# Performance work log

Measured on AMD Instinct MI355X. Metric: run time of the kernel, lower is better.

Reference implementation:

```python
import jax, jax.numpy as jnp
import numpy as np
import math

B, H, L, DK = 4, 12, 1024, 64
GLOBAL, LOCAL, INIT_VAL = 8, 4, 8
W = INIT_VAL + 1  # window length fed to each GRU
MAX_VAL = 1.0e12


def setup_inputs() -> dict:
    k0 = jax.random.key(0)
    ks = jax.random.split(k0, 9)
    bound = 1.0 / math.sqrt(DK)
    uni = lambda k, shape: jax.random.uniform(k, shape, jnp.float32, -bound, bound)
    return {
        "query": jax.random.normal(ks[0], (B, H, L, DK), jnp.float32),
        "key": jax.random.normal(ks[1], (B, H, L, DK), jnp.float32),
        "value": jax.random.normal(ks[2], (B, H, L, DK), jnp.float32),
        "mask": jax.random.randint(ks[3], (B, 1, L, L), 0, 2, jnp.int32),
        # per-local-head GRU parameters (torch nn.GRU layout: gates [r, z, n])
        "w_ih": uni(ks[4], (LOCAL, 3 * DK, DK)),
        "w_hh": uni(ks[5], (LOCAL, 3 * DK, DK)),
        "b_ih": uni(ks[6], (LOCAL, 3 * DK)),
        "b_hh": uni(ks[7], (LOCAL, 3 * DK)),
    }


def reference(query, key, value, mask, w_ih, w_hh, b_ih, b_hh):
    b, h, l, d_k = query.shape
    # ---- global softmax-attention heads ----
    q_g, k_g, v_g = query[:, :GLOBAL], key[:, :GLOBAL], value[:, :GLOBAL]
    scores = jnp.einsum('bhqd,bhkd->bhqk', q_g, k_g) / math.sqrt(d_k)
    scores = jnp.where(mask == 0, -MAX_VAL, scores)
    p_attn = jax.nn.softmax(scores, axis=-1)
    out_g = jnp.einsum('bhqk,bhkd->bhqd', p_attn, v_g)  # (b, GLOBAL, l, d_k)

    # ---- local heads: windowed value gather ----
    v_l = value[:, GLOBAL:]                                   # (b, LOCAL, l, d_k)
    v_pad = jnp.pad(v_l, ((0, 0), (0, 0), (0, INIT_VAL), (0, 0)))
    dist = jnp.arange(l)[:, None] + jnp.arange(W)[None, :]    # (l, W) forward window
    v_aug = v_pad[:, :, dist, :]                              # (b, LOCAL, l, W, d_k)
    x = v_aug.reshape(b * LOCAL * l, W, d_k)                  # all windows, shared by every GRU

    # ---- per-head GRU over the window; keep last hidden state ----
    def gru_last_hidden(wih, whh, bih, bhh):
        xg = jnp.einsum('ntd,gd->ntg', x, wih) + bih          # (N, W, 3*d_k), input gates precomputed
        def step(hc, xg_t):
            gh = hc @ whh.T + bhh
            xr, xz, xn = jnp.split(xg_t, 3, axis=-1)
            hr, hz, hn = jnp.split(gh, 3, axis=-1)
            r = jax.nn.sigmoid(xr + hr)
            z = jax.nn.sigmoid(xz + hz)
            n_ = jnp.tanh(xn + r * hn)
            return (1.0 - z) * n_ + z * hc, None
        h0 = jnp.zeros((x.shape[0], d_k), x.dtype)
        hT, _ = jax.lax.scan(step, h0, jnp.swapaxes(xg, 0, 1))
        return hT                                             # (N, d_k)

    hs = jax.vmap(gru_last_hidden)(w_ih, w_hh, b_ih, b_hh)    # (LOCAL, N, d_k)
    # faithful to torch cat: GRU i applied to ALL local heads -> LOCAL*LOCAL output heads
    out_l = hs.reshape(LOCAL, b, LOCAL, l, d_k).transpose(1, 0, 2, 3, 4)
    out_l = out_l.reshape(b, LOCAL * LOCAL, l, d_k)

    return jnp.concatenate([out_g, out_l], axis=1)            # (b, GLOBAL + LOCAL^2, l, d_k)
```

## Files before the change

kernel.cpp:

```cpp
#include <hip/hip_runtime.h>

#define B_  4
#define H_  12
#define L_  1024
#define DK_ 64
#define GH_ 8
#define WS_ 9

#define ATTN_LDS_BYTES (3 * 64 * 64 * 2)
#define GRU_W_OFF    0
#define GRU_XGT_OFF  24576
#define GRU_HB_OFF   81408
#define GRU_BIH_OFF  114176
#define GRU_LDS_BYTES 114944
#define XGT_STRIDE   296

#define MB_WORDS (B_ * L_ * 16)

typedef __attribute__((ext_vector_type(8))) short short8;
typedef __attribute__((ext_vector_type(4))) float f32x4;

#define MFMA_BF16(a, b, c) __builtin_amdgcn_mfma_f32_16x16x32_bf16((a), (b), (c), 0, 0, 0)

__device__ __forceinline__ unsigned short f2bf(float f) {
  unsigned int u = __builtin_bit_cast(unsigned int, f);
  u += 0x7fffu + ((u >> 16) & 1u);
  return (unsigned short)(u >> 16);
}
__device__ __forceinline__ float bf2f(unsigned short s) {
  return __builtin_bit_cast(float, ((unsigned int)s) << 16);
}
__device__ __forceinline__ short8 pack8(const float4 a, const float4 b) {
  short8 r;
  r[0] = (short)f2bf(a.x); r[1] = (short)f2bf(a.y);
  r[2] = (short)f2bf(a.z); r[3] = (short)f2bf(a.w);
  r[4] = (short)f2bf(b.x); r[5] = (short)f2bf(b.y);
  r[6] = (short)f2bf(b.z); r[7] = (short)f2bf(b.w);
  return r;
}
__device__ __forceinline__ uint4 packrow16(const float4 a, const float4 b) {
  uint4 r;
  r.x = (unsigned)f2bf(a.x) | ((unsigned)f2bf(a.y) << 16);
  r.y = (unsigned)f2bf(a.z) | ((unsigned)f2bf(a.w) << 16);
  r.z = (unsigned)f2bf(b.x) | ((unsigned)f2bf(b.y) << 16);
  r.w = (unsigned)f2bf(b.z) | ((unsigned)f2bf(b.w) << 16);
  return r;
}
__device__ __forceinline__ float xg_get(const uint2* xg3, const int wi) {
  const unsigned d = (wi & 2) ? xg3[wi >> 2].y : xg3[wi >> 2].x;
  return (wi & 1) ? __builtin_bit_cast(float, d & 0xffff0000u)
                  : __builtin_bit_cast(float, d << 16);
}

__global__ __launch_bounds__(256) void maskpack_kernel(
    const int* __restrict__ mask, unsigned long long* __restrict__ mb)
{
  const int idx = blockIdx.x * 256 + threadIdx.x;
  const int* src = mask + (size_t)idx * 64;
  unsigned long long bits = 0ull;
#pragma unroll
  for (int i = 0; i < 16; ++i) {
    const int4 m4 = *(const int4*)(src + i * 4);
    if (m4.x) bits |= 1ull << (i * 4 + 0);
    if (m4.y) bits |= 1ull << (i * 4 + 1);
    if (m4.z) bits |= 1ull << (i * 4 + 2);
    if (m4.w) bits |= 1ull << (i * 4 + 3);
  }
  mb[idx] = bits;
}

__global__ __launch_bounds__(256) void attn_kernel(
    const float* __restrict__ q, const float* __restrict__ k,
    const float* __restrict__ v, const int* __restrict__ mask,
    const unsigned long long* __restrict__ mb, const int use_bits,
    float* __restrict__ out)
{
  extern __shared__ char smc[];
  char* sK  = smc;
  char* sVT = smc + 8192;
  char* sP  = smc + 16384;

  const int tid = threadIdx.x;
  const int q0 = blockIdx.x * 64;
  const int h  = blockIdx.y;
  const int b  = blockIdx.z;

  const int w  = tid >> 6;
  const int ln = tid & 63;
  const int lg = ln >> 4;
  const int c  = ln & 15;

  const size_t hbase = ((size_t)b * H_ + h) * L_ * DK_;
  const float* kp = k + hbase;
  const float* vp = v + hbase;
  const int*   mp = mask + (size_t)b * L_ * L_;
  const unsigned long long* mbp = mb + (size_t)b * L_ * 16;

  short8 qa[2];
  {
    const float* qrow = q + hbase + (size_t)(q0 + w * 16 + c) * DK_ + lg * 8;
#pragma unroll
    for (int kt = 0; kt < 2; ++kt) {
      const float4 f0 = *(const float4*)(qrow + kt * 32);
      const float4 f1 = *(const float4*)(qrow + kt * 32 + 4);
      qa[kt] = pack8(f0, f1);
    }
  }

  char* sPw = sP + w * 2048;

  f32x4 o_[4];
#pragma unroll
  for (int nt = 0; nt < 4; ++nt) { o_[nt][0] = 0.f; o_[nt][1] = 0.f; o_[nt][2] = 0.f; o_[nt][3] = 0.f; }
  float mrun[4], lrun[4];
#pragma unroll
  for (int r = 0; r < 4; ++r) { mrun[r] = -1e30f; lrun[r] = 0.f; }

  const int rr  = tid >> 2;
  const int c16 = (tid & 3) << 4;

  float4 kreg[4], vreg[4];
  unsigned long long mreg[4];
  {
    const float* ksrc = kp + (size_t)rr * DK_ + c16;
    kreg[0] = *(const float4*)(ksrc);      kreg[1] = *(const float4*)(ksrc + 4);
    kreg[2] = *(const float4*)(ksrc + 8);  kreg[3] = *(const float4*)(ksrc + 12);
    const float* vsrc = vp + (size_t)rr * DK_ + c16;
    vreg[0] = *(const float4*)(vsrc);      vreg[1] = *(const float4*)(vsrc + 4);
    vreg[2] = *(const float4*)(vsrc + 8);  vreg[3] = *(const float4*)(vsrc + 12);
    if (use_bits) {
#pragma unroll
      for (int r = 0; r < 4; ++r)
        mreg[r] = mbp[(size_t)(q0 + w * 16 + lg * 4 + r) * 16 + 0];
    }
  }

  for (int kt0 = 0; kt0 < 16; ++kt0) {
    {
      const int kb = rr * 128 + c16 * 2;
      const int sw = (rr & 7) << 4;
      *(uint4*)(sK + ((kb) ^ sw))      = packrow16(kreg[0], kreg[1]);
      *(uint4*)(sK + ((kb + 16) ^ sw)) = packrow16(kreg[2], kreg[3]);
      const float vv[16] = {vreg[0].x, vreg[0].y, vreg[0].z, vreg[0].w,
                            vreg[1].x, vreg[1].y, vreg[1].z, vreg[1].w,
                            vreg[2].x, vreg[2].y, vreg[2].z, vreg[2].w,
                            vreg[3].x, vreg[3].y, vreg[3].z, vreg[3].w};
#pragma unroll
      for (int j = 0; j < 16; ++j) {
        const int d = c16 + j;
        *(unsigned short*)(sVT + ((d * 128 + rr * 2) ^ ((d & 7) << 4))) = f2bf(vv[j]);
      }
    }
    __syncthreads();

    unsigned long long mcur[4];
#pragma unroll
    for (int r = 0; r < 4; ++r) mcur[r] = mreg[r];
    {
      const int ktn = (kt0 + 1) & 15;
      const float* ksrc = kp + (size_t)(ktn * 64 + rr) * DK_ + c16;
      kreg[0] = *(const float4*)(ksrc);      kreg[1] = *(const float4*)(ksrc + 4);
      kreg[2] = *(const float4*)(ksrc + 8);  kreg[3] = *(const float4*)(ksrc + 12);
      const float* vsrc = vp + (size_t)(ktn * 64 + rr) * DK_ + c16;
      vreg[0] = *(const float4*)(vsrc);      vreg[1] = *(const float4*)(vsrc + 4);
      vreg[2] = *(const float4*)(vsrc + 8);  vreg[3] = *(const float4*)(vsrc + 12);
      if (use_bits) {
#pragma unroll
        for (int r = 0; r < 4; ++r)
          mreg[r] = mbp[(size_t)(q0 + w * 16 + lg * 4 + r) * 16 + ktn];
      }
    }

    f32x4 acc[4];
#pragma unroll
    for (int nt = 0; nt < 4; ++nt) {
      acc[nt][0] = 0.f; acc[nt][1] = 0.f; acc[nt][2] = 0.f; acc[nt][3] = 0.f;
#pragma unroll
      for (int kt = 0; kt < 2; ++kt) {
        const int off = (((nt * 16 + c) * 128 + kt * 64 + lg * 16) ^ ((c & 7) << 4));
        const short8 bk = __builtin_bit_cast(short8, *(const uint4*)(sK + off));
        acc[nt] = MFMA_BF16(qa[kt], bk, acc[nt]);
      }
    }

#pragma unroll
    for (int r = 0; r < 4; ++r) {
      bool k0_, k1_, k2_, k3_;
      if (use_bits) {
        const unsigned long long mword = mcur[r];
        k0_ = (mword >> (c)) & 1ull;
        k1_ = (mword >> (16 + c)) & 1ull;
        k2_ = (mword >> (32 + c)) & 1ull;
        k3_ = (mword >> (48 + c)) & 1ull;
      } else {
        const int qr = q0 + w * 16 + lg * 4 + r;
        const int* mrow = mp + (size_t)qr * L_ + kt0 * 64 + c;
        k0_ = mrow[0] != 0; k1_ = mrow[16] != 0; k2_ = mrow[32] != 0; k3_ = mrow[48] != 0;
      }
      const float s0_ = k0_ ? acc[0][r] * 0.125f : -1e12f;
      const float s1_ = k1_ ? acc[1][r] * 0.125f : -1e12f;
      const float s2_ = k2_ ? acc[2][r] * 0.125f : -1e12f;
      const float s3_ = k3_ ? acc[3][r] * 0.125f : -1e12f;
      float mt = fmaxf(fmaxf(s0_, s1_), fmaxf(s2_, s3_));
#pragma unroll
      for (int off = 1; off < 16; off <<= 1) mt = fmaxf(mt, __shfl_xor(mt, off));
      const float mnew = fmaxf(mrun[r], mt);
      const float p0 = __expf(s0_ - mnew);
      const float p1 = __expf(s1_ - mnew);
      const float p2 = __expf(s2_ - mnew);
      const float p3 = __expf(s3_ - mnew);
      float pt = p0 + p1 + p2 + p3;
#pragma unroll
      for (int off = 1; off < 16; off <<= 1) pt += __shfl_xor(pt, off);
      const float scale = __expf(mrun[r] - mnew);
      mrun[r] = mnew;
      lrun[r] = lrun[r] * scale + pt;
      o_[0][r] *= scale; o_[1][r] *= scale; o_[2][r] *= scale; o_[3][r] *= scale;
      const int prow = lg * 4 + r;
      const int pb = prow * 128;
      const int psw = (prow & 7) << 4;
      *(unsigned short*)(sPw + ((pb + (c * 2)) ^ psw))       = f2bf(p0);
      *(unsigned short*)(sPw + ((pb + (16 + c) * 2) ^ psw))  = f2bf(p1);
      *(unsigned short*)(sPw + ((pb + (32 + c) * 2) ^ psw))  = f2bf(p2);
      *(unsigned short*)(sPw + ((pb + (48 + c) * 2) ^ psw))  = f2bf(p3);
    }

#pragma unroll
    for (int kt = 0; kt < 2; ++kt) {
      const int aoff = ((c * 128 + kt * 64 + lg * 16) ^ ((c & 7) << 4));
      const short8 pa = __builtin_bit_cast(short8, *(const uint4*)(sPw + aoff));
#pragma unroll
      for (int nt = 0; nt < 4; ++nt) {
        const int boff = (((nt * 16 + c) * 128 + kt * 64 + lg * 16) ^ ((c & 7) << 4));
        const short8 bv = __builtin_bit_cast(short8, *(const uint4*)(sVT + boff));
        o_[nt] = MFMA_BF16(pa, bv, o_[nt]);
      }
    }
    __syncthreads();
  }

  float* op = out + (((size_t)b * 24 + h) * L_ + q0 + w * 16) * DK_;
#pragma unroll
  for (int r = 0; r < 4; ++r) {
    const float inv = 1.f / lrun[r];
#pragma unroll
    for (int nt = 0; nt < 4; ++nt)
      op[(size_t)(lg * 4 + r) * DK_ + nt * 16 + c] = o_[nt][r] * inv;
  }
}

__global__ __launch_bounds__(512) void gru_kernel(
    const float* __restrict__ value, const float* __restrict__ wih_g,
    const float* __restrict__ whh_g, const float* __restrict__ bih_g,
    const float* __restrict__ bhh_g, float* __restrict__ out)
{
  extern __shared__ char smc[];
  char*  sW   = smc + GRU_W_OFF;
  char*  sXGT = smc + GRU_XGT_OFF;
  char*  sHB  = smc + GRU_HB_OFF;
  float* sBih = (float*)(smc + GRU_BIH_OFF);

  const int tid  = threadIdx.x;
  const int l0   = blockIdx.x * 128;
  const int gset = blockIdx.y >> 2;
  const int vh   = blockIdx.y & 3;
  const int b    = blockIdx.z;

  const float* vp   = value + (((size_t)b * H_ + GH_ + vh) * L_) * DK_;
  const float* wih  = wih_g + (size_t)gset * 192 * DK_;
  const float* whh  = whh_g + (size_t)gset * 192 * DK_;
  const float* bihp = bih_g + gset * 192;
  const float* bhhp = bhh_g + gset * 192;

  if (tid < 192) sBih[tid] = bihp[tid];
#pragma unroll
  for (int k2 = 0; k2 < 4; ++k2) {
    uint4 z; z.x = 0u; z.y = 0u; z.z = 0u; z.w = 0u;
    *(uint4*)(sHB + ((size_t)tid + 512 * k2) * 16) = z;
  }
  for (int cid = tid; cid < 1536; cid += 512) {
    const int row = cid >> 3, ch = cid & 7;
    const float* wp = whh + row * 64 + ch * 8;
    const float4 w0 = *(const float4*)wp;
    const float4 w1 = *(const float4*)(wp + 4);
    *(uint4*)(sW + ((row * 128 + ch * 16) ^ ((row & 7) << 4))) = packrow16(w0, w1);
  }
  __syncthreads();

  const int w  = tid >> 6;
  const int ln = tid & 63;
  const int lg = ln >> 4;
  const int c  = ln & 15;

  for (int t = w; t < 108; t += 8) {
    const int Mt = t / 12, Nt = t - Mt * 12;
    const int row = l0 + Mt * 16 + c;
    const bool valid = row < L_;
    const float* va = vp + (size_t)row * 64 + lg * 8;
    float4 z4; z4.x = 0.f; z4.y = 0.f; z4.z = 0.f; z4.w = 0.f;
    const float4 a00 = valid ? *(const float4*)(va)      : z4;
    const float4 a01 = valid ? *(const float4*)(va + 4)  : z4;
    const float4 a10 = valid ? *(const float4*)(va + 32) : z4;
    const float4 a11 = valid ? *(const float4*)(va + 36) : z4;
    const float* wb = wih + (size_t)(Nt * 16 + c) * 64 + lg * 8;
    const float4 b00 = *(const float4*)(wb);
    const float4 b01 = *(const float4*)(wb + 4);
    const float4 b10 = *(const float4*)(wb + 32);
    const float4 b11 = *(const float4*)(wb + 36);
    f32x4 acc = {0.f, 0.f, 0.f, 0.f};
    acc = MFMA_BF16(pack8(a00, a01), pack8(b00, b01), acc);
    acc = MFMA_BF16(pack8(a10, a11), pack8(b10, b11), acc);
    const float bias = sBih[Nt * 16 + c];
    const int pos0 = Mt * 16 + lg * 4;
    const int jj = Nt * 16 + c;
    uint2 pk;
    pk.x = (unsigned)f2bf(acc[0] + bias) | ((unsigned)f2bf(acc[1] + bias) << 16);
    pk.y = (unsigned)f2bf(acc[2] + bias) | ((unsigned)f2bf(acc[3] + bias) << 16);
    *(uint2*)(sXGT + jj * XGT_STRIDE + pos0 * 2) = pk;
  }
  __syncthreads();

  char* hbH = sHB + w * 4096;
  char* hbL = hbH + 2048;
  const int seqB = w * 16;

  float bhh[12];
#pragma unroll
  for (int n = 0; n < 12; ++n) bhh[n] = bhhp[n * 16 + c];

  const int P0 = seqB + lg * 4;
  uint2 xgq[4][3][3];
#pragma unroll
  for (int t = 0; t < 4; ++t)
#pragma unroll
    for (int g = 0; g < 3; ++g) {
      const char* rowp = sXGT + (g * 64 + t * 16 + c) * XGT_STRIDE + P0 * 2;
#pragma unroll
      for (int kk = 0; kk < 3; ++kk)
        xgq[t][g][kk] = *(const uint2*)(rowp + kk * 8);
    }

  f32x4 hfr[4];
#pragma unroll
  for (int t = 0; t < 4; ++t) { hfr[t][0] = 0.f; hfr[t][1] = 0.f; hfr[t][2] = 0.f; hfr[t][3] = 0.f; }

#pragma unroll
  for (int ts = 0; ts < WS_; ++ts) {
    short8 ahi[2], alo[2];
#pragma unroll
    for (int kt = 0; kt < 2; ++kt) {
      const int ao = (c * 128 + kt * 64 + lg * 16) ^ ((c & 7) << 4);
      ahi[kt] = __builtin_bit_cast(short8, *(const uint4*)(hbH + ao));
      alo[kt] = __builtin_bit_cast(short8, *(const uint4*)(hbL + ao));
    }
    f32x4 acc[12];
#pragma unroll
    for (int n = 0; n < 12; ++n) {
      acc[n][0] = 0.f; acc[n][1] = 0.f; acc[n][2] = 0.f; acc[n][3] = 0.f;
#pragma unroll
      for (int kt = 0; kt < 2; ++kt) {
        const int wo = ((n * 16 + c) * 128 + kt * 64 + lg * 16) ^ ((c & 7) << 4);
        const short8 bw = __builtin_bit_cast(short8, *(const uint4*)(sW + wo));
        acc[n] = MFMA_BF16(ahi[kt], bw, acc[n]);
        acc[n] = MFMA_BF16(alo[kt], bw, acc[n]);
      }
    }
#pragma unroll
    for (int t = 0; t < 4; ++t) {
#pragma unroll
      for (int r = 0; r < 4; ++r) {
        const int wi = r + ts;
        const float xr = xg_get(xgq[t][0], wi);
        const float xz = xg_get(xgq[t][1], wi);
        const float xn = xg_get(xgq[t][2], wi);
        const float ghr = acc[t][r] + bhh[t];
        const float ghz = acc[t + 4][r] + bhh[t + 4];
        const float ghn = acc[t + 8][r] + bhh[t + 8];
        const float rr = __builtin_amdgcn_rcpf(1.f + __expf(-(xr + ghr)));
        const float zz = __builtin_amdgcn_rcpf(1.f + __expf(-(xz + ghz)));
        const float e2 = __expf(2.f * (xn + rr * ghn));
        const float nn = 1.f - 2.f * __builtin_amdgcn_rcpf(1.f + e2);
        float h = hfr[t][r];
        h = (1.f - zz) * nn + zz * h;
        hfr[t][r] = h;
        const int sl = lg * 4 + r;
        const int d = c + 16 * t;
        const int hb = (sl * 128 + d * 2) ^ ((sl & 7) << 4);
        const unsigned short hhi = f2bf(h);
        *(unsigned short*)(hbH + hb) = hhi;
        *(unsigned short*)(hbL + hb) = f2bf(h - bf2f(hhi));
      }
    }
  }

  float* op = out + (((size_t)b * 24 + (GH_ + gset * 4 + vh)) * L_ + l0) * DK_;
#pragma unroll
  for (int t = 0; t < 4; ++t)
#pragma unroll
    for (int r = 0; r < 4; ++r)
      op[(size_t)(seqB + lg * 4 + r) * 64 + c + 16 * t] = hfr[t][r];
}

extern "C" void kernel_launch(void* const* d_in, const int* in_sizes, int n_in,
                              void* d_out, int out_size, void* d_ws, size_t ws_size,
                              hipStream_t stream) {
  (void)in_sizes; (void)n_in; (void)out_size;
  const float* q   = (const float*)d_in[0];
  const float* k   = (const float*)d_in[1];
  const float* v   = (const float*)d_in[2];
  const int*   msk = (const int*)d_in[3];
  const float* wih = (const float*)d_in[4];
  const float* whh = (const float*)d_in[5];
  const float* bih = (const float*)d_in[6];
  const float* bhh = (const float*)d_in[7];
  float* out = (float*)d_out;

  const int use_bits = (ws_size >= (size_t)MB_WORDS * 8) ? 1 : 0;
  unsigned long long* mb = (unsigned long long*)d_ws;

  (void)hipFuncSetAttribute((const void*)gru_kernel,
                            hipFuncAttributeMaxDynamicSharedMemorySize, GRU_LDS_BYTES);

  if (use_bits)
    maskpack_kernel<<<dim3(MB_WORDS / 256), dim3(256), 0, stream>>>(msk, mb);
  attn_kernel<<<dim3(L_ / 64, GH_, B_), dim3(256), ATTN_LDS_BYTES, stream>>>(
      q, k, v, msk, mb, use_bits, out);
  gru_kernel<<<dim3(L_ / 128, 16, B_), dim3(512), GRU_LDS_BYTES, stream>>>(
      v, wih, whh, bih, bhh, out);
}
```

Measured before the change: 325.9 us.

## Keep GRU hidden state in registers via permuted weight rows, trim LDS

The GRU recurrence now uses a transposed MFMA formulation. W_hh rows are permuted so that each lane's output fragment directly forms the next step's B operand. This removes the per-step LDS round trip for the hidden state, shrinks LDS so more blocks fit per CU (launch bounds 512,4), folds b_hh for the r/z gates into the precomputed input gates, and skips the first step's matmul since h0 is zero. The attention kernel also packs V transposed stores into 32-bit writes and replaces __syncthreads with a waitcnt plus a raw barrier. The risks are the added index complexity and possible register pressure from the occupancy hint.

```diff
diff --git a/kernel.cpp b/kernel.cpp
--- a/kernel.cpp
+++ b/kernel.cpp
@@ -9,11 +9,11 @@
 
 #define ATTN_LDS_BYTES (3 * 64 * 64 * 2)
 #define GRU_W_OFF    0
-#define GRU_XGT_OFF  24576
-#define GRU_HB_OFF   81408
-#define GRU_BIH_OFF  114176
-#define GRU_LDS_BYTES 114944
-#define XGT_STRIDE   296
+#define GRU_XGP_OFF  24576
+#define GRU_BIH_OFF  77888
+#define GRU_BHH_OFF  78656
+#define GRU_LDS_BYTES 79424
+#define XGP_STRIDE   392
 
 #define MB_WORDS (B_ * L_ * 16)
 
@@ -46,10 +46,13 @@
   r.w = (unsigned)f2bf(b.z) | ((unsigned)f2bf(b.w) << 16);
   return r;
 }
-__device__ __forceinline__ float xg_get(const uint2* xg3, const int wi) {
-  const unsigned d = (wi & 2) ? xg3[wi >> 2].y : xg3[wi >> 2].x;
-  return (wi & 1) ? __builtin_bit_cast(float, d & 0xffff0000u)
-                  : __builtin_bit_cast(float, d << 16);
+__device__ __forceinline__ float bfget(const uint2 u, const int r) {
+  const unsigned d = (r & 2) ? u.y : u.x;
+  return (r & 1) ? __builtin_bit_cast(float, d & 0xffff0000u)
+                 : __builtin_bit_cast(float, d << 16);
+}
+__device__ __forceinline__ int pi_row(const int dt, const int m) {
+  return ((dt & 1) << 5) + ((m >> 2) << 3) + ((dt >> 1) << 2) + (m & 3);
 }
 
 __global__ __launch_bounds__(256) void maskpack_kernel(
@@ -118,6 +121,8 @@
 
   const int rr  = tid >> 2;
   const int c16 = (tid & 3) << 4;
+  const int r2  = (tid & 31) << 1;
+  const int j0v = (tid >> 5) << 3;
 
   float4 kreg[4], vreg[4];
   unsigned long long mreg[4];
@@ -125,9 +130,9 @@
     const float* ksrc = kp + (size_t)rr * DK_ + c16;
     kreg[0] = *(const float4*)(ksrc);      kreg[1] = *(const float4*)(ksrc + 4);
     kreg[2] = *(const float4*)(ksrc + 8);  kreg[3] = *(const float4*)(ksrc + 12);
-    const float* vsrc = vp + (size_t)rr * DK_ + c16;
-    vreg[0] = *(const float4*)(vsrc);      vreg[1] = *(const float4*)(vsrc + 4);
-    vreg[2] = *(const float4*)(vsrc + 8);  vreg[3] = *(const float4*)(vsrc + 12);
+    const float* vsrc = vp + (size_t)r2 * DK_ + j0v;
+    vreg[0] = *(const float4*)(vsrc);       vreg[1] = *(const float4*)(vsrc + 4);
+    vreg[2] = *(const float4*)(vsrc + 64);  vreg[3] = *(const float4*)(vsrc + 68);
     if (use_bits) {
 #pragma unroll
       for (int r = 0; r < 4; ++r)
@@ -141,17 +146,19 @@
       const int sw = (rr & 7) << 4;
       *(uint4*)(sK + ((kb) ^ sw))      = packrow16(kreg[0], kreg[1]);
       *(uint4*)(sK + ((kb + 16) ^ sw)) = packrow16(kreg[2], kreg[3]);
-      const float vv[16] = {vreg[0].x, vreg[0].y, vreg[0].z, vreg[0].w,
-                            vreg[1].x, vreg[1].y, vreg[1].z, vreg[1].w,
-                            vreg[2].x, vreg[2].y, vreg[2].z, vreg[2].w,
+      const float va_[8] = {vreg[0].x, vreg[0].y, vreg[0].z, vreg[0].w,
+                            vreg[1].x, vreg[1].y, vreg[1].z, vreg[1].w};
+      const float vb_[8] = {vreg[2].x, vreg[2].y, vreg[2].z, vreg[2].w,
                             vreg[3].x, vreg[3].y, vreg[3].z, vreg[3].w};
 #pragma unroll
-      for (int j = 0; j < 16; ++j) {
-        const int d = c16 + j;
-        *(unsigned short*)(sVT + ((d * 128 + rr * 2) ^ ((d & 7) << 4))) = f2bf(vv[j]);
-      }
-    }
-    __syncthreads();
+      for (int j = 0; j < 8; ++j) {
+        const int d = j0v + j;
+        const unsigned u32v = (unsigned)f2bf(va_[j]) | ((unsigned)f2bf(vb_[j]) << 16);
+        *(unsigned*)(sVT + ((d * 128 + r2 * 2) ^ ((d & 7) << 4))) = u32v;
+      }
+    }
+    asm volatile("s_waitcnt lgkmcnt(0)" ::: "memory");
+    __builtin_amdgcn_s_barrier();
 
     unsigned long long mcur[4];
 #pragma unroll
@@ -161,9 +168,9 @@
       const float* ksrc = kp + (size_t)(ktn * 64 + rr) * DK_ + c16;
       kreg[0] = *(const float4*)(ksrc);      kreg[1] = *(const float4*)(ksrc + 4);
       kreg[2] = *(const float4*)(ksrc + 8);  kreg[3] = *(const float4*)(ksrc + 12);
-      const float* vsrc = vp + (size_t)(ktn * 64 + rr) * DK_ + c16;
-      vreg[0] = *(const float4*)(vsrc);      vreg[1] = *(const float4*)(vsrc + 4);
-      vreg[2] = *(const float4*)(vsrc + 8);  vreg[3] = *(const float4*)(vsrc + 12);
+      const float* vsrc = vp + (size_t)(ktn * 64 + r2) * DK_ + j0v;
+      vreg[0] = *(const float4*)(vsrc);       vreg[1] = *(const float4*)(vsrc + 4);
+      vreg[2] = *(const float4*)(vsrc + 64);  vreg[3] = *(const float4*)(vsrc + 68);
       if (use_bits) {
 #pragma unroll
         for (int r = 0; r < 4; ++r)
@@ -236,7 +243,8 @@
         o_[nt] = MFMA_BF16(pa, bv, o_[nt]);
       }
     }
-    __syncthreads();
+    asm volatile("s_waitcnt lgkmcnt(0)" ::: "memory");
+    __builtin_amdgcn_s_barrier();
   }
 
   float* op = out + (((size_t)b * 24 + h) * L_ + q0 + w * 16) * DK_;
@@ -249,16 +257,16 @@
   }
 }
 
-__global__ __launch_bounds__(512) void gru_kernel(
+__global__ __launch_bounds__(512, 4) void gru_kernel(
     const float* __restrict__ value, const float* __restrict__ wih_g,
     const float* __restrict__ whh_g, const float* __restrict__ bih_g,
     const float* __restrict__ bhh_g, float* __restrict__ out)
 {
   extern __shared__ char smc[];
   char*  sW   = smc + GRU_W_OFF;
-  char*  sXGT = smc + GRU_XGT_OFF;
-  char*  sHB  = smc + GRU_HB_OFF;
+  char*  sXGP = smc + GRU_XGP_OFF;
   float* sBih = (float*)(smc + GRU_BIH_OFF);
+  float* sBhh = (float*)(smc + GRU_BHH_OFF);
 
   const int tid  = threadIdx.x;
   const int l0   = blockIdx.x * 128;
@@ -272,15 +280,13 @@
   const float* bihp = bih_g + gset * 192;
   const float* bhhp = bhh_g + gset * 192;
 
-  if (tid < 192) sBih[tid] = bihp[tid];
-#pragma unroll
-  for (int k2 = 0; k2 < 4; ++k2) {
-    uint4 z; z.x = 0u; z.y = 0u; z.z = 0u; z.w = 0u;
-    *(uint4*)(sHB + ((size_t)tid + 512 * k2) * 16) = z;
-  }
+  if (tid < 192) { sBih[tid] = bihp[tid]; sBhh[tid] = bhhp[tid]; }
+
   for (int cid = tid; cid < 1536; cid += 512) {
     const int row = cid >> 3, ch = cid & 7;
-    const float* wp = whh + row * 64 + ch * 8;
+    const int g = row >> 6, dt = (row >> 4) & 3, m = row & 15;
+    const int arow = g * 64 + pi_row(dt, m);
+    const float* wp = whh + (size_t)arow * 64 + ch * 8;
     const float4 w0 = *(const float4*)wp;
     const float4 w1 = *(const float4*)(wp + 4);
     *(uint4*)(sW + ((row * 128 + ch * 16) ^ ((row & 7) << 4))) = packrow16(w0, w1);
@@ -293,112 +299,122 @@
   const int c  = ln & 15;
 
   for (int t = w; t < 108; t += 8) {
-    const int Mt = t / 12, Nt = t - Mt * 12;
-    const int row = l0 + Mt * 16 + c;
-    const bool valid = row < L_;
-    const float* va = vp + (size_t)row * 64 + lg * 8;
+    const int jt = t % 12, pt = t / 12;
+    const int g = jt >> 2, dt = jt & 3;
+    const int aj = g * 64 + pi_row(dt, c);
+    const float* wb = wih + (size_t)aj * 64 + lg * 8;
+    const short8 aA = pack8(*(const float4*)(wb),      *(const float4*)(wb + 4));
+    const short8 aB = pack8(*(const float4*)(wb + 32), *(const float4*)(wb + 36));
+    const int pos = pt * 16 + c;
+    const int gp  = l0 + pos;
+    const bool valid = gp < L_;
     float4 z4; z4.x = 0.f; z4.y = 0.f; z4.z = 0.f; z4.w = 0.f;
-    const float4 a00 = valid ? *(const float4*)(va)      : z4;
-    const float4 a01 = valid ? *(const float4*)(va + 4)  : z4;
-    const float4 a10 = valid ? *(const float4*)(va + 32) : z4;
-    const float4 a11 = valid ? *(const float4*)(va + 36) : z4;
-    const float* wb = wih + (size_t)(Nt * 16 + c) * 64 + lg * 8;
-    const float4 b00 = *(const float4*)(wb);
-    const float4 b01 = *(const float4*)(wb + 4);
-    const float4 b10 = *(const float4*)(wb + 32);
-    const float4 b11 = *(const float4*)(wb + 36);
+    const float* va = vp + (size_t)gp * 64 + lg * 8;
+    const short8 bA = pack8(valid ? *(const float4*)(va)      : z4,
+                            valid ? *(const float4*)(va + 4)  : z4);
+    const short8 bB = pack8(valid ? *(const float4*)(va + 32) : z4,
+                            valid ? *(const float4*)(va + 36) : z4);
     f32x4 acc = {0.f, 0.f, 0.f, 0.f};
-    acc = MFMA_BF16(pack8(a00, a01), pack8(b00, b01), acc);
-    acc = MFMA_BF16(pack8(a10, a11), pack8(b10, b11), acc);
-    const float bias = sBih[Nt * 16 + c];
-    const int pos0 = Mt * 16 + lg * 4;
-    const int jj = Nt * 16 + c;
-    uint2 pk;
-    pk.x = (unsigned)f2bf(acc[0] + bias) | ((unsigned)f2bf(acc[1] + bias) << 16);
-    pk.y = (unsigned)f2bf(acc[2] + bias) | ((unsigned)f2bf(acc[3] + bias) << 16);
-    *(uint2*)(sXGT + jj * XGT_STRIDE + pos0 * 2) = pk;
+    acc = MFMA_BF16(aA, bA, acc);
+    acc = MFMA_BF16(aB, bB, acc);
+    const int jb = g * 64 + ((dt & 1) << 5) + (lg << 3) + ((dt >> 1) << 2);
+    const f32x4 bi = *(const f32x4*)(sBih + jb);
+    const f32x4 bh4 = *(const f32x4*)(sBhh + jb);
+    const float foldh = (g < 2) ? 1.f : 0.f;
+    if (pos < 136) {
+      uint2 pk;
+      pk.x = (unsigned)f2bf(acc[0] + bi[0] + foldh * bh4[0]) |
+             ((unsigned)f2bf(acc[1] + bi[1] + foldh * bh4[1]) << 16);
+      pk.y = (unsigned)f2bf(acc[2] + bi[2] + foldh * bh4[2]) |
+             ((unsigned)f2bf(acc[3] + bi[3] + foldh * bh4[3]) << 16);
+      *(uint2*)(sXGP + pos * XGP_STRIDE + jt * 32 + lg * 8) = pk;
+    }
   }
   __syncthreads();
 
-  char* hbH = sHB + w * 4096;
-  char* hbL = hbH + 2048;
   const int seqB = w * 16;
-
-  float bhh[12];
-#pragma unroll
-  for (int n = 0; n < 12; ++n) bhh[n] = bhhp[n * 16 + c];
-
-  const int P0 = seqB + lg * 4;
-  uint2 xgq[4][3][3];
-#pragma unroll
-  for (int t = 0; t < 4; ++t)
-#pragma unroll
-    for (int g = 0; g < 3; ++g) {
-      const char* rowp = sXGT + (g * 64 + t * 16 + c) * XGT_STRIDE + P0 * 2;
-#pragma unroll
-      for (int kk = 0; kk < 3; ++kk)
-        xgq[t][g][kk] = *(const uint2*)(rowp + kk * 8);
-    }
-
-  f32x4 hfr[4];
-#pragma unroll
-  for (int t = 0; t < 4; ++t) { hfr[t][0] = 0.f; hfr[t][1] = 0.f; hfr[t][2] = 0.f; hfr[t][3] = 0.f; }
+  const int xrow0 = seqB + c;
+
+  f32x4 bhn[4];
+#pragma unroll
+  for (int dt = 0; dt < 4; ++dt)
+    bhn[dt] = *(const f32x4*)(sBhh + 128 + ((dt & 1) << 5) + (lg << 3) + ((dt >> 1) << 2));
+
+  float hfr[4][4];
+#pragma unroll
+  for (int dt = 0; dt < 4; ++dt)
+#pragma unroll
+    for (int r = 0; r < 4; ++r) hfr[dt][r] = 0.f;
+
+  short8 bh[2], bl[2];
 
 #pragma unroll
   for (int ts = 0; ts < WS_; ++ts) {
-    short8 ahi[2], alo[2];
-#pragma unroll
-    for (int kt = 0; kt < 2; ++kt) {
-      const int ao = (c * 128 + kt * 64 + lg * 16) ^ ((c & 7) << 4);
-      ahi[kt] = __builtin_bit_cast(short8, *(const uint4*)(hbH + ao));
-      alo[kt] = __builtin_bit_cast(short8, *(const uint4*)(hbL + ao));
-    }
+    uint2 xg[12];
+#pragma unroll
+    for (int jt = 0; jt < 12; ++jt)
+      xg[jt] = *(const uint2*)(sXGP + (xrow0 + ts) * XGP_STRIDE + jt * 32 + lg * 8);
+
     f32x4 acc[12];
-#pragma unroll
-    for (int n = 0; n < 12; ++n) {
-      acc[n][0] = 0.f; acc[n][1] = 0.f; acc[n][2] = 0.f; acc[n][3] = 0.f;
+    if (ts == 0) {
+#pragma unroll
+      for (int jt = 0; jt < 12; ++jt) {
+        acc[jt][0] = 0.f; acc[jt][1] = 0.f; acc[jt][2] = 0.f; acc[jt][3] = 0.f;
+      }
+    } else {
+#pragma unroll
+      for (int jt = 0; jt < 12; ++jt) {
+        acc[jt][0] = 0.f; acc[jt][1] = 0.f; acc[jt][2] = 0.f; acc[jt][3] = 0.f;
+#pragma unroll
+        for (int kt = 0; kt < 2; ++kt) {
+          const int wo = (((jt * 16 + c) * 128 + kt * 64 + lg * 16) ^ ((c & 7) << 4));
+          const short8 wv = __builtin_bit_cast(short8, *(const uint4*)(sW + wo));
+          acc[jt] = MFMA_BF16(wv, bh[kt], acc[jt]);
+          acc[jt] = MFMA_BF16(wv, bl[kt], acc[jt]);
+        }
+      }
+    }
+
+#pragma unroll
+    for (int dt = 0; dt < 4; ++dt) {
+#pragma unroll
+      for (int r = 0; r < 4; ++r) {
+        const float xr = bfget(xg[dt], r);
+        const float xz = bfget(xg[4 + dt], r);
+        const float xn = bfget(xg[8 + dt], r);
+        const float rr_ = __builtin_amdgcn_rcpf(1.f + __expf(-(xr + acc[dt][r])));
+        const float zz  = __builtin_amdgcn_rcpf(1.f + __expf(-(xz + acc[4 + dt][r])));
+        const float hn  = acc[8 + dt][r] + bhn[dt][r];
+        const float e2  = __expf(2.f * (xn + rr_ * hn));
+        const float nn  = 1.f - 2.f * __builtin_amdgcn_rcpf(1.f + e2);
+        hfr[dt][r] = (1.f - zz) * nn + zz * hfr[dt][r];
+      }
+    }
+
+    if (ts < WS_ - 1) {
 #pragma unroll
       for (int kt = 0; kt < 2; ++kt) {
-        const int wo = ((n * 16 + c) * 128 + kt * 64 + lg * 16) ^ ((c & 7) << 4);
-        const short8 bw = __builtin_bit_cast(short8, *(const uint4*)(sW + wo));
-        acc[n] = MFMA_BF16(ahi[kt], bw, acc[n]);
-        acc[n] = MFMA_BF16(alo[kt], bw, acc[n]);
-      }
-    }
-#pragma unroll
-    for (int t = 0; t < 4; ++t) {
-#pragma unroll
-      for (int r = 0; r < 4; ++r) {
-        const int wi = r + ts;
-        const float xr = xg_get(xgq[t][0], wi);
-        const float xz = xg_get(xgq[t][1], wi);
-        const float xn = xg_get(xgq[t][2], wi);
-        const float ghr = acc[t][r] + bhh[t];
-        const float ghz = acc[t + 4][r] + bhh[t + 4];
-        const float ghn = acc[t + 8][r] + bhh[t + 8];
-        const float rr = __builtin_amdgcn_rcpf(1.f + __expf(-(xr + ghr)));
-        const float zz = __builtin_amdgcn_rcpf(1.f + __expf(-(xz + ghz)));
-        const float e2 = __expf(2.f * (xn + rr * ghn));
-        const float nn = 1.f - 2.f * __builtin_amdgcn_rcpf(1.f + e2);
-        float h = hfr[t][r];
-        h = (1.f - zz) * nn + zz * h;
-        hfr[t][r] = h;
-        const int sl = lg * 4 + r;
-        const int d = c + 16 * t;
-        const int hb = (sl * 128 + d * 2) ^ ((sl & 7) << 4);
-        const unsigned short hhi = f2bf(h);
-        *(unsigned short*)(hbH + hb) = hhi;
-        *(unsigned short*)(hbL + hb) = f2bf(h - bf2f(hhi));
-      }
-    }
-  }
-
-  float* op = out + (((size_t)b * 24 + (GH_ + gset * 4 + vh)) * L_ + l0) * DK_;
-#pragma unroll
-  for (int t = 0; t < 4; ++t)
-#pragma unroll
-    for (int r = 0; r < 4; ++r)
-      op[(size_t)(seqB + lg * 4 + r) * 64 + c + 16 * t] = hfr[t][r];
+        short8 hi8, lo8;
+#pragma unroll
+        for (int i = 0; i < 8; ++i) {
+          const float hv = (i < 4) ? hfr[kt][i] : hfr[kt + 2][i - 4];
+          const unsigned short hb16 = f2bf(hv);
+          hi8[i] = (short)hb16;
+          lo8[i] = (short)f2bf(hv - bf2f(hb16));
+        }
+        bh[kt] = hi8; bl[kt] = lo8;
+      }
+    }
+  }
+
+  float* op = out + (((size_t)b * 24 + (GH_ + gset * 4 + vh)) * L_ + l0 + seqB + c) * DK_;
+#pragma unroll
+  for (int dt = 0; dt < 4; ++dt)
+#pragma unroll
+    for (int r = 0; r < 4; ++r) {
+      const int dact = ((dt & 1) << 5) + (lg << 3) + ((dt >> 1) << 2) + r;
+      op[dact] = hfr[dt][r];
+    }
 }
 
 extern "C" void kernel_launch(void* const* d_in, const int* in_sizes, int n_in,
```

After: 431.7 us. +32.5%, slower.
